# Kernel tuning notes

Hardware: AMD Instinct MI355X
Metric: run time of the kernel (lower is better)

Reference implementation:

```python
import jax, jax.numpy as jnp
import numpy as np

B, N, H = 2, 2048, 256
NUM_HEADS = 8
HEAD_DIM = H // NUM_HEADS
E = 65536
NEG = -1e30
LN_EPS = 1e-5


def setup_inputs() -> dict:
    key = jax.random.key(0)
    ks = jax.random.split(key, 8)
    x = jax.random.normal(ks[0], (B, N, H), dtype=jnp.float32)
    edge_index = jax.random.randint(ks[1], (2, E), 0, N, dtype=jnp.int32)
    edge_weights = jax.random.uniform(ks[2], (E,), dtype=jnp.float32)
    s = 1.0 / np.sqrt(H)
    Wq = jax.random.normal(ks[3], (H, H), dtype=jnp.float32) * s
    Wk = jax.random.normal(ks[4], (H, H), dtype=jnp.float32) * s
    Wv = jax.random.normal(ks[5], (H, H), dtype=jnp.float32) * s
    Wo = jax.random.normal(ks[6], (H, H), dtype=jnp.float32) * s
    ln_gamma = jnp.ones((H,), dtype=jnp.float32)
    ln_beta = jnp.zeros((H,), dtype=jnp.float32)
    return {"node_embeddings": x, "edge_index": edge_index, "edge_weights": edge_weights,
            "Wq": Wq, "Wk": Wk, "Wv": Wv, "Wo": Wo, "ln_gamma": ln_gamma, "ln_beta": ln_beta}


def reference(node_embeddings, edge_index, edge_weights, Wq, Wk, Wv, Wo, ln_gamma, ln_beta):
    x = node_embeddings
    residual = x
    # torch Linear: y = x @ W.T
    def proj(W):
        y = jnp.einsum('bnd,ed->bne', x, W)
        return y.reshape(B, N, NUM_HEADS, HEAD_DIM).transpose(0, 2, 1, 3)  # [B,h,N,hd]
    Q, K, V = proj(Wq), proj(Wk), proj(Wv)
    scale = 1.0 / jnp.sqrt(jnp.float32(HEAD_DIM))
    scores = jnp.einsum('bhnd,bhmd->bhnm', Q, K) * scale  # [B,h,N,N]
    # adjacency mask from edge list
    mask = jnp.zeros((N, N), dtype=bool).at[edge_index[0], edge_index[1]].set(True)
    scores = jnp.where(mask[None, None], scores, NEG)
    w = jax.nn.softmax(scores, axis=-1)
    # rows with no edges: softmax over uniform NEG -> uniform; multiply by mask zeroes them
    # (equivalent to torch's -inf softmax + nan->0, but grad-safe)
    w = w * mask[None, None].astype(w.dtype)
    attn = jnp.einsum('bhnm,bhmd->bhnd', w, V)
    attn = attn.transpose(0, 2, 1, 3).reshape(B, N, H)
    out = jnp.einsum('bnd,ed->bne', attn, Wo)
    y = out + residual
    mu = jnp.mean(y, axis=-1, keepdims=True)
    var = jnp.mean(jnp.square(y - mu), axis=-1, keepdims=True)
    y = (y - mu) / jnp.sqrt(var + LN_EPS) * ln_gamma + ln_beta
    return y
```

## Files before the change

kernel.cpp:

```cpp
#include <hip/hip_runtime.h>
#include <math.h>

#define Bb 2
#define Nn 2048
#define Hh 256
#define NH 8
#define HD 32
#define NEDGE 65536
#define LN_EPS 1e-5f
#define MW 64
#define LDA2 72
#define ALD 264
#define NBW 2112

typedef __bf16 bf16_t;
typedef bf16_t bf16x8 __attribute__((ext_vector_type(8)));
typedef bf16_t bf16x4 __attribute__((ext_vector_type(4)));
typedef float f32x4 __attribute__((ext_vector_type(4)));

__global__ __launch_bounds__(256) void prep_kernel(
    const float* __restrict__ x,
    const float* __restrict__ Wq, const float* __restrict__ Wk, const float* __restrict__ Wv,
    const int* __restrict__ ei,
    float* __restrict__ Qb, bf16_t* __restrict__ Kb16, bf16_t* __restrict__ Vb16,
    unsigned int* __restrict__ mask)
{
    __shared__ bf16_t As[64 * LDA2];
    __shared__ bf16_t Ws[64 * LDA2];
    const int u = blockIdx.x;
    const int t = threadIdx.x;

    if (u >= 768) {
        int e = (u - 768) * 256 + t;
        int src = ei[e];
        int dst = ei[NEDGE + e];
        atomicOr(&mask[src * MW + (dst >> 5)], 1u << (dst & 31));
        return;
    }

    const int lane = t & 63, w = t >> 6;
    const int wm = w & 1, wn = w >> 1;
    const int ml = lane & 15, quad = lane >> 4;
    const int m0 = (u & 63) << 6;
    const int ysel = u >> 6;
    const int wsel = ysel >> 2;
    const float* W = (wsel == 0) ? Wq : ((wsel == 1) ? Wk : Wv);
    const int n0 = (ysel & 3) << 6;
    const int srow = t >> 3, scol = (t & 7) * 8;
    f32x4 acc[2][2];
    f32x4 zero = {0.f, 0.f, 0.f, 0.f};
    acc[0][0] = zero; acc[0][1] = zero; acc[1][0] = zero; acc[1][1] = zero;

    for (int k0 = 0; k0 < Hh; k0 += 64) {
        float4 a[2][2], bwt[2][2];
        #pragma unroll
        for (int s = 0; s < 2; ++s) {
            const float* ap = x + (size_t)(m0 + srow + s * 32) * Hh + k0 + scol;
            a[s][0] = *(const float4*)ap;
            a[s][1] = *(const float4*)(ap + 4);
            const float* bp = W + (size_t)(n0 + srow + s * 32) * Hh + k0 + scol;
            bwt[s][0] = *(const float4*)bp;
            bwt[s][1] = *(const float4*)(bp + 4);
        }
        __syncthreads();
        #pragma unroll
        for (int s = 0; s < 2; ++s) {
            bf16x8 av = {(bf16_t)a[s][0].x, (bf16_t)a[s][0].y, (bf16_t)a[s][0].z, (bf16_t)a[s][0].w,
                         (bf16_t)a[s][1].x, (bf16_t)a[s][1].y, (bf16_t)a[s][1].z, (bf16_t)a[s][1].w};
            bf16x8 bv = {(bf16_t)bwt[s][0].x, (bf16_t)bwt[s][0].y, (bf16_t)bwt[s][0].z, (bf16_t)bwt[s][0].w,
                         (bf16_t)bwt[s][1].x, (bf16_t)bwt[s][1].y, (bf16_t)bwt[s][1].z, (bf16_t)bwt[s][1].w};
            *(bf16x8*)&As[(srow + s * 32) * LDA2 + scol] = av;
            *(bf16x8*)&Ws[(srow + s * 32) * LDA2 + scol] = bv;
        }
        __syncthreads();
        #pragma unroll
        for (int kk = 0; kk < 64; kk += 32) {
            bf16x8 af[2], bfr[2];
            #pragma unroll
            for (int i = 0; i < 2; ++i) {
                af[i]  = *(const bf16x8*)&As[(wm * 32 + i * 16 + ml) * LDA2 + kk + quad * 8];
                bfr[i] = *(const bf16x8*)&Ws[(wn * 32 + i * 16 + ml) * LDA2 + kk + quad * 8];
            }
            #pragma unroll
            for (int i = 0; i < 2; ++i)
                #pragma unroll
                for (int j = 0; j < 2; ++j)
                    acc[i][j] = __builtin_amdgcn_mfma_f32_16x16x32_bf16(af[i], bfr[j], acc[i][j], 0, 0, 0);
        }
    }
    bf16_t* Ob16 = (wsel == 1) ? Kb16 : Vb16;
    #pragma unroll
    for (int i = 0; i < 2; ++i)
        #pragma unroll
        for (int j = 0; j < 2; ++j)
            #pragma unroll
            for (int r = 0; r < 4; ++r) {
                int mg = m0 + wm * 32 + i * 16 + quad * 4 + r;
                int ng = n0 + wn * 32 + j * 16 + ml;
                float v = acc[i][j][r];
                if (wsel == 0) Qb[(size_t)mg * Hh + ng] = v;
                else           Ob16[(size_t)mg * Hh + ng] = (bf16_t)v;
            }
}

__global__ __launch_bounds__(1024) void attn_out_ln_kernel(
    const float* __restrict__ Qb, const bf16_t* __restrict__ Kb16, const bf16_t* __restrict__ Vb16,
    const unsigned int* __restrict__ mask, const float* __restrict__ Wo,
    const float* __restrict__ x, const float* __restrict__ gamma, const float* __restrict__ beta,
    float* __restrict__ out)
{
    __shared__ __align__(16) char smem[16 * NBW * 2 + 16 * ALD * 2 + 256 * LDA2 * 2];
    unsigned short* nbr = (unsigned short*)smem;
    float*  ybuf = (float*)smem;
    bf16_t* As   = (bf16_t*)(smem + 16 * NBW * 2);
    bf16_t* Ws   = (bf16_t*)(smem + 16 * NBW * 2 + 16 * ALD * 2);

    const int t = threadIdx.x;
    const int w = t >> 6, lane = t & 63;
    const int ml = lane & 15, quad = lane >> 4;
    const int g = (blockIdx.x << 4) + w;
    const int i = g & (Nn - 1);
    const int b = g >> 11;

    unsigned int bits = mask[i * MW + lane];
    int cnt = __popc(bits);
    int incl = cnt;
    #pragma unroll
    for (int off = 1; off < 64; off <<= 1) {
        int v = __shfl_up(incl, off, 64);
        if (lane >= off) incl += v;
    }
    int idx = incl - cnt;
    unsigned int bb = bits;
    while (bb) {
        int bit = __ffs(bb) - 1;
        nbr[w * NBW + idx++] = (unsigned short)(lane * 32 + bit);
        bb &= bb - 1;
    }
    int nn = __shfl(incl, 63, 64);
    if (lane == 63) nbr[w * NBW + idx] = 0;
    __syncthreads();

    const int off4 = lane << 2;
    const float4 qv = *(const float4*)(Qb + (size_t)g * Hh + off4);
    const bf16_t* kb = Kb16 + ((size_t)b << 19);
    const bf16_t* vb = Vb16 + ((size_t)b << 19);
    const float scale = 0.17677669529663687f;

    float m_run = -1e30f, l_run = 0.f;
    float o0 = 0.f, o1 = 0.f, o2 = 0.f, o3 = 0.f;
    if (nn > 0) {
        int j = nbr[w * NBW];
        bf16x4 kv = *(const bf16x4*)(kb + ((size_t)j << 8) + off4);
        bf16x4 vv = *(const bf16x4*)(vb + ((size_t)j << 8) + off4);
        for (int n = 0; n < nn; ++n) {
            int jn = nbr[w * NBW + n + 1];
            bf16x4 kn = *(const bf16x4*)(kb + ((size_t)jn << 8) + off4);
            bf16x4 vn = *(const bf16x4*)(vb + ((size_t)jn << 8) + off4);
            float p = fmaf((float)kv.x, qv.x, fmaf((float)kv.y, qv.y,
                      fmaf((float)kv.z, qv.z, (float)kv.w * qv.w)));
            p += __shfl_xor(p, 1, 64);
            p += __shfl_xor(p, 2, 64);
            p += __shfl_xor(p, 4, 64);
            p *= scale;
            float m_new = fmaxf(m_run, p);
            float alpha = __expf(m_run - m_new);
            float wgt   = __expf(p - m_new);
            l_run = fmaf(l_run, alpha, wgt);
            o0 = fmaf(o0, alpha, wgt * (float)vv.x);
            o1 = fmaf(o1, alpha, wgt * (float)vv.y);
            o2 = fmaf(o2, alpha, wgt * (float)vv.z);
            o3 = fmaf(o3, alpha, wgt * (float)vv.w);
            m_run = m_new;
            kv = kn; vv = vn;
        }
    }
    float linv = (l_run > 0.f) ? 1.f / l_run : 0.f;
    bf16x4 arow = {(bf16_t)(o0 * linv), (bf16_t)(o1 * linv),
                   (bf16_t)(o2 * linv), (bf16_t)(o3 * linv)};
    *(bf16x4*)&As[w * ALD + off4] = arow;
    __syncthreads();

    const int wrow = t >> 2, wcol = (t & 3) << 4;
    f32x4 acc = {0.f, 0.f, 0.f, 0.f};
    for (int k0 = 0; k0 < Hh; k0 += 64) {
        const float* wp = Wo + (size_t)wrow * Hh + k0 + wcol;
        float4 w0 = ((const float4*)wp)[0];
        float4 w1 = ((const float4*)wp)[1];
        float4 w2 = ((const float4*)wp)[2];
        float4 w3 = ((const float4*)wp)[3];
        __syncthreads();
        bf16x8 lo = {(bf16_t)w0.x, (bf16_t)w0.y, (bf16_t)w0.z, (bf16_t)w0.w,
                     (bf16_t)w1.x, (bf16_t)w1.y, (bf16_t)w1.z, (bf16_t)w1.w};
        bf16x8 hi = {(bf16_t)w2.x, (bf16_t)w2.y, (bf16_t)w2.z, (bf16_t)w2.w,
                     (bf16_t)w3.x, (bf16_t)w3.y, (bf16_t)w3.z, (bf16_t)w3.w};
        *(bf16x8*)&Ws[wrow * LDA2 + wcol] = lo;
        *(bf16x8*)&Ws[wrow * LDA2 + wcol + 8] = hi;
        __syncthreads();
        #pragma unroll
        for (int kk = 0; kk < 64; kk += 32) {
            bf16x8 af  = *(const bf16x8*)&As[ml * ALD + k0 + kk + quad * 8];
            bf16x8 bfr = *(const bf16x8*)&Ws[(w * 16 + ml) * LDA2 + kk + quad * 8];
            acc = __builtin_amdgcn_mfma_f32_16x16x32_bf16(af, bfr, acc, 0, 0, 0);
        }
    }
    #pragma unroll
    for (int r = 0; r < 4; ++r) {
        int row = quad * 4 + r;
        int col = (w << 4) + ml;
        ybuf[row * 260 + col] = acc[r] + x[(size_t)((blockIdx.x << 4) + row) * Hh + col];
    }
    __syncthreads();
    {
        float4 v = *(const float4*)&ybuf[w * 260 + off4];
        float sum = v.x + v.y + v.z + v.w;
        #pragma unroll
        for (int m = 1; m < 64; m <<= 1) sum += __shfl_xor(sum, m, 64);
        float mu = sum * (1.f / Hh);
        float4 d = {v.x - mu, v.y - mu, v.z - mu, v.w - mu};
        float ss = d.x * d.x + d.y * d.y + d.z * d.z + d.w * d.w;
        #pragma unroll
        for (int m = 1; m < 64; m <<= 1) ss += __shfl_xor(ss, m, 64);
        float r = rsqrtf(ss * (1.f / Hh) + LN_EPS);
        float4 gm = *(const float4*)(gamma + off4);
        float4 bt = *(const float4*)(beta + off4);
        float4 ov = {d.x * r * gm.x + bt.x, d.y * r * gm.y + bt.y,
                     d.z * r * gm.z + bt.z, d.w * r * gm.w + bt.w};
        *(float4*)(out + (size_t)g * Hh + off4) = ov;
    }
}

extern "C" void kernel_launch(void* const* d_in, const int* in_sizes, int n_in,
                              void* d_out, int out_size, void* d_ws, size_t ws_size,
                              hipStream_t stream) {
    const float* x     = (const float*)d_in[0];
    const int*   ei    = (const int*)d_in[1];
    const float* Wq    = (const float*)d_in[3];
    const float* Wk    = (const float*)d_in[4];
    const float* Wv    = (const float*)d_in[5];
    const float* Wo    = (const float*)d_in[6];
    const float* gamma = (const float*)d_in[7];
    const float* beta  = (const float*)d_in[8];
    float* out = (float*)d_out;

    const int NTOK = Bb * Nn * Hh;
    float*  Qb    = (float*)d_ws;
    bf16_t* Kb16  = (bf16_t*)(Qb + NTOK);
    bf16_t* Vb16  = Kb16 + NTOK;
    unsigned int* mask = (unsigned int*)(Vb16 + NTOK);

    hipMemsetAsync(mask, 0, Nn * MW * sizeof(unsigned int), stream);
    hipLaunchKernelGGL(prep_kernel, dim3(1024), dim3(256), 0, stream,
                       x, Wq, Wk, Wv, ei, Qb, Kb16, Vb16, mask);
    hipLaunchKernelGGL(attn_out_ln_kernel, dim3((Bb * Nn) / 16), dim3(1024), 0, stream,
                       Qb, Kb16, Vb16, mask, Wo, x, gamma, beta, out);
}
```

Baseline: 110.3 us.

## Split attention into two interleaved softmax streams and shrink blocks to 8 rows

The online-softmax loop over neighbours now keeps two independent accumulators (even and odd edges), prefetching two edges ahead, and merges them at the end. This shortens the serial dependency chain and raises memory-level parallelism. Blocks drop from 16 rows and 1024 threads to 8 rows and 512 threads, using less shared memory so more blocks can fit per CU. The Wo projection now reads Wo straight from global memory into MFMA fragments instead of staging it in LDS, wasting half of each 16-row MFMA tile on zero rows and re-reading Wo per block.

```diff
diff --git a/kernel.cpp b/kernel.cpp
--- a/kernel.cpp
+++ b/kernel.cpp
@@ -103,22 +103,21 @@
             }
 }
 
-__global__ __launch_bounds__(1024) void attn_out_ln_kernel(
+__global__ __launch_bounds__(512, 4) void attn_fused2_kernel(
     const float* __restrict__ Qb, const bf16_t* __restrict__ Kb16, const bf16_t* __restrict__ Vb16,
     const unsigned int* __restrict__ mask, const float* __restrict__ Wo,
     const float* __restrict__ x, const float* __restrict__ gamma, const float* __restrict__ beta,
     float* __restrict__ out)
 {
-    __shared__ __align__(16) char smem[16 * NBW * 2 + 16 * ALD * 2 + 256 * LDA2 * 2];
+    __shared__ __align__(16) char smem[8 * NBW * 2 + 8 * ALD * 2];
     unsigned short* nbr = (unsigned short*)smem;
     float*  ybuf = (float*)smem;
-    bf16_t* As   = (bf16_t*)(smem + 16 * NBW * 2);
-    bf16_t* Ws   = (bf16_t*)(smem + 16 * NBW * 2 + 16 * ALD * 2);
+    bf16_t* As   = (bf16_t*)(smem + 8 * NBW * 2);
 
     const int t = threadIdx.x;
     const int w = t >> 6, lane = t & 63;
     const int ml = lane & 15, quad = lane >> 4;
-    const int g = (blockIdx.x << 4) + w;
+    const int g = (blockIdx.x << 3) + w;
     const int i = g & (Nn - 1);
     const int b = g >> 11;
 
@@ -138,7 +137,11 @@
         bb &= bb - 1;
     }
     int nn = __shfl(incl, 63, 64);
-    if (lane == 63) nbr[w * NBW + idx] = 0;
+    if (lane == 63) {
+        nbr[w * NBW + idx]     = 0;
+        nbr[w * NBW + idx + 1] = 0;
+        nbr[w * NBW + idx + 2] = 0;
+    }
     __syncthreads();
 
     const int off4 = lane << 2;
@@ -147,68 +150,102 @@
     const bf16_t* vb = Vb16 + ((size_t)b << 19);
     const float scale = 0.17677669529663687f;
 
-    float m_run = -1e30f, l_run = 0.f;
-    float o0 = 0.f, o1 = 0.f, o2 = 0.f, o3 = 0.f;
+    float m_e = -1e30f, l_e = 0.f, e0 = 0.f, e1 = 0.f, e2 = 0.f, e3 = 0.f;
+    float m_o = -1e30f, l_o = 0.f, d0 = 0.f, d1 = 0.f, d2 = 0.f, d3 = 0.f;
     if (nn > 0) {
-        int j = nbr[w * NBW];
-        bf16x4 kv = *(const bf16x4*)(kb + ((size_t)j << 8) + off4);
-        bf16x4 vv = *(const bf16x4*)(vb + ((size_t)j << 8) + off4);
-        for (int n = 0; n < nn; ++n) {
-            int jn = nbr[w * NBW + n + 1];
-            bf16x4 kn = *(const bf16x4*)(kb + ((size_t)jn << 8) + off4);
-            bf16x4 vn = *(const bf16x4*)(vb + ((size_t)jn << 8) + off4);
-            float p = fmaf((float)kv.x, qv.x, fmaf((float)kv.y, qv.y,
-                      fmaf((float)kv.z, qv.z, (float)kv.w * qv.w)));
-            p += __shfl_xor(p, 1, 64);
-            p += __shfl_xor(p, 2, 64);
-            p += __shfl_xor(p, 4, 64);
-            p *= scale;
-            float m_new = fmaxf(m_run, p);
-            float alpha = __expf(m_run - m_new);
-            float wgt   = __expf(p - m_new);
-            l_run = fmaf(l_run, alpha, wgt);
-            o0 = fmaf(o0, alpha, wgt * (float)vv.x);
-            o1 = fmaf(o1, alpha, wgt * (float)vv.y);
-            o2 = fmaf(o2, alpha, wgt * (float)vv.z);
-            o3 = fmaf(o3, alpha, wgt * (float)vv.w);
-            m_run = m_new;
-            kv = kn; vv = vn;
-        }
-    }
-    float linv = (l_run > 0.f) ? 1.f / l_run : 0.f;
+        const unsigned short* nb = &nbr[w * NBW];
+        int j0 = nb[0], j1 = nb[1];
+        bf16x4 kve = *(const bf16x4*)(kb + ((size_t)j0 << 8) + off4);
+        bf16x4 vve = *(const bf16x4*)(vb + ((size_t)j0 << 8) + off4);
+        bf16x4 kvo = *(const bf16x4*)(kb + ((size_t)j1 << 8) + off4);
+        bf16x4 vvo = *(const bf16x4*)(vb + ((size_t)j1 << 8) + off4);
+        for (int n = 0; n < nn; n += 2) {
+            int j2 = nb[n + 2], j3 = nb[n + 3];
+            bf16x4 kne = *(const bf16x4*)(kb + ((size_t)j2 << 8) + off4);
+            bf16x4 vne = *(const bf16x4*)(vb + ((size_t)j2 << 8) + off4);
+            bf16x4 kno = *(const bf16x4*)(kb + ((size_t)j3 << 8) + off4);
+            bf16x4 vno = *(const bf16x4*)(vb + ((size_t)j3 << 8) + off4);
+            {
+                float p = fmaf((float)kve.x, qv.x, fmaf((float)kve.y, qv.y,
+                          fmaf((float)kve.z, qv.z, (float)kve.w * qv.w)));
+                p += __shfl_xor(p, 1, 64);
+                p += __shfl_xor(p, 2, 64);
+                p += __shfl_xor(p, 4, 64);
+                p *= scale;
+                float mn = fmaxf(m_e, p);
+                float al = __expf(m_e - mn);
+                float wg = __expf(p - mn);
+                l_e = fmaf(l_e, al, wg);
+                e0 = fmaf(e0, al, wg * (float)vve.x);
+                e1 = fmaf(e1, al, wg * (float)vve.y);
+                e2 = fmaf(e2, al, wg * (float)vve.z);
+                e3 = fmaf(e3, al, wg * (float)vve.w);
+                m_e = mn;
+            }
+            if (n + 1 < nn) {
+                float p = fmaf((float)kvo.x, qv.x, fmaf((float)kvo.y, qv.y,
+                          fmaf((float)kvo.z, qv.z, (float)kvo.w * qv.w)));
+                p += __shfl_xor(p, 1, 64);
+                p += __shfl_xor(p, 2, 64);
+                p += __shfl_xor(p, 4, 64);
+                p *= scale;
+                float mn = fmaxf(m_o, p);
+                float al = __expf(m_o - mn);
+                float wg = __expf(p - mn);
+                l_o = fmaf(l_o, al, wg);
+                d0 = fmaf(d0, al, wg * (float)vvo.x);
+                d1 = fmaf(d1, al, wg * (float)vvo.y);
+                d2 = fmaf(d2, al, wg * (float)vvo.z);
+                d3 = fmaf(d3, al, wg * (float)vvo.w);
+                m_o = mn;
+            }
+            kve = kne; vve = vne; kvo = kno; vvo = vno;
+        }
+    }
+    float mm = fmaxf(m_e, m_o);
+    float se = __expf(m_e - mm);
+    float so = __expf(m_o - mm);
+    float l  = fmaf(l_e, se, l_o * so);
+    float o0 = fmaf(e0, se, d0 * so);
+    float o1 = fmaf(e1, se, d1 * so);
+    float o2 = fmaf(e2, se, d2 * so);
+    float o3 = fmaf(e3, se, d3 * so);
+    float linv = (l > 0.f) ? 1.f / l : 0.f;
     bf16x4 arow = {(bf16_t)(o0 * linv), (bf16_t)(o1 * linv),
                    (bf16_t)(o2 * linv), (bf16_t)(o3 * linv)};
     *(bf16x4*)&As[w * ALD + off4] = arow;
     __syncthreads();
 
-    const int wrow = t >> 2, wcol = (t & 3) << 4;
-    f32x4 acc = {0.f, 0.f, 0.f, 0.f};
-    for (int k0 = 0; k0 < Hh; k0 += 64) {
-        const float* wp = Wo + (size_t)wrow * Hh + k0 + wcol;
-        float4 w0 = ((const float4*)wp)[0];
-        float4 w1 = ((const float4*)wp)[1];
-        float4 w2 = ((const float4*)wp)[2];
-        float4 w3 = ((const float4*)wp)[3];
-        __syncthreads();
-        bf16x8 lo = {(bf16_t)w0.x, (bf16_t)w0.y, (bf16_t)w0.z, (bf16_t)w0.w,
-                     (bf16_t)w1.x, (bf16_t)w1.y, (bf16_t)w1.z, (bf16_t)w1.w};
-        bf16x8 hi = {(bf16_t)w2.x, (bf16_t)w2.y, (bf16_t)w2.z, (bf16_t)w2.w,
-                     (bf16_t)w3.x, (bf16_t)w3.y, (bf16_t)w3.z, (bf16_t)w3.w};
-        *(bf16x8*)&Ws[wrow * LDA2 + wcol] = lo;
-        *(bf16x8*)&Ws[wrow * LDA2 + wcol + 8] = hi;
-        __syncthreads();
-        #pragma unroll
-        for (int kk = 0; kk < 64; kk += 32) {
-            bf16x8 af  = *(const bf16x8*)&As[ml * ALD + k0 + kk + quad * 8];
-            bf16x8 bfr = *(const bf16x8*)&Ws[(w * 16 + ml) * LDA2 + kk + quad * 8];
-            acc = __builtin_amdgcn_mfma_f32_16x16x32_bf16(af, bfr, acc, 0, 0, 0);
-        }
-    }
+    f32x4 acc[2];
+    {
+        f32x4 pz = {0.f, 0.f, 0.f, 0.f};
+        acc[0] = pz; acc[1] = pz;
+    }
+    const bf16x8 zero8 = {(bf16_t)0.f, (bf16_t)0.f, (bf16_t)0.f, (bf16_t)0.f,
+                          (bf16_t)0.f, (bf16_t)0.f, (bf16_t)0.f, (bf16_t)0.f};
     #pragma unroll
-    for (int r = 0; r < 4; ++r) {
-        int row = quad * 4 + r;
-        int col = (w << 4) + ml;
-        ybuf[row * 260 + col] = acc[r] + x[(size_t)((blockIdx.x << 4) + row) * Hh + col];
+    for (int k8 = 0; k8 < 8; ++k8) {
+        bf16x8 af = zero8;
+        if (ml < 8) af = *(const bf16x8*)&As[ml * ALD + (k8 << 5) + (quad << 3)];
+        #pragma unroll
+        for (int ct = 0; ct < 2; ++ct) {
+            const float* wp = Wo + (size_t)((w << 5) + (ct << 4) + ml) * Hh + (k8 << 5) + (quad << 3);
+            float4 w0 = ((const float4*)wp)[0];
+            float4 w1 = ((const float4*)wp)[1];
+            bf16x8 bfr = {(bf16_t)w0.x, (bf16_t)w0.y, (bf16_t)w0.z, (bf16_t)w0.w,
+                          (bf16_t)w1.x, (bf16_t)w1.y, (bf16_t)w1.z, (bf16_t)w1.w};
+            acc[ct] = __builtin_amdgcn_mfma_f32_16x16x32_bf16(af, bfr, acc[ct], 0, 0, 0);
+        }
+    }
+    if (quad < 2) {
+        #pragma unroll
+        for (int ct = 0; ct < 2; ++ct)
+            #pragma unroll
+            for (int r = 0; r < 4; ++r) {
+                int row = quad * 4 + r;
+                int col = (w << 5) + (ct << 4) + ml;
+                ybuf[row * 260 + col] = acc[ct][r] + x[(size_t)((blockIdx.x << 3) + row) * Hh + col];
+            }
     }
     __syncthreads();
     {
@@ -252,6 +289,6 @@
     hipMemsetAsync(mask, 0, Nn * MW * sizeof(unsigned int), stream);
     hipLaunchKernelGGL(prep_kernel, dim3(1024), dim3(256), 0, stream,
                        x, Wq, Wk, Wv, ei, Qb, Kb16, Vb16, mask);
-    hipLaunchKernelGGL(attn_out_ln_kernel, dim3((Bb * Nn) / 16), dim3(1024), 0, stream,
+    hipLaunchKernelGGL(attn_fused2_kernel, dim3((Bb * Nn) / 8), dim3(512), 0, stream,
                        Qb, Kb16, Vb16, mask, Wo, x, gamma, beta, out);
 }
```

Result: no change. 110.9 us (+0.5%).
